# Kernel optimization log

Hardware: AMD Instinct MI355X
Metric: run time of the kernel (lower is better)

## Reference

```python
import jax, jax.numpy as jnp
import numpy as np

LN_EPS = 1e-5

def sin_emb(coords, dim):
    # coords [..., 3] -> [..., dim]; dim split evenly over 3 axes, sin/cos halves
    per_axis = dim // 3
    half = per_axis // 2
    freqs = jnp.exp(-jnp.log(10000.0) * jnp.arange(half, dtype=coords.dtype) / max(half - 1, 1))
    ang = coords[..., None] * freqs  # [..., 3, half]
    emb = jnp.concatenate([jnp.sin(ang), jnp.cos(ang)], axis=-1)  # [..., 3, per_axis]
    return emb.reshape(coords.shape[:-1] + (dim,))

def layernorm(x, g, b):
    mu = jnp.mean(x, axis=-1, keepdims=True)
    var = jnp.mean((x - mu) ** 2, axis=-1, keepdims=True)
    return (x - mu) * jax.lax.rsqrt(var + LN_EPS) * g + b

def point_mlp(x, w, b, g, be, act):
    h = layernorm(x @ w + b, g, be)
    return jax.nn.gelu(h, approximate=False) if act else h

def query_ball_point(radius, nsample, xyz):
    # xyz [B,N,3] -> idx [B,N,nsample] (pad with first in-ball index, PointNet++ style)
    N = xyz.shape[1]
    sq = jnp.sum((xyz[:, :, None, :] - xyz[:, None, :, :]) ** 2, axis=-1)  # [B,N,N]
    idx0 = jnp.where(sq > radius * radius, N, jnp.arange(N)[None, None, :])
    idx = jnp.sort(idx0, axis=-1)[:, :, :nsample]
    return jnp.where(idx == N, idx[:, :, :1], idx)

def index_points(points, idx):
    # points [B,N,C], idx [B,S,K] -> [B,S,K,C]
    return jax.vmap(lambda p, i: p[i])(points, idx)

def setup_inputs() -> dict:
    key = jax.random.key(0)
    ks = jax.random.split(key, 20)
    B, N, C_stem, C_tok = 4, 4096, 64, 256
    C_in = C_stem + 3 + 24 + 96  # 187
    w = lambda k, i, o: jax.random.normal(k, (i, o), jnp.float32) * 0.02
    inp = {
        'xyz': jax.random.uniform(ks[0], (B, N, 3), jnp.float32),
        'point_feature': jax.random.normal(ks[1], (B, N, C_stem), jnp.float32),
        # scene_point_mlp
        'w1': w(ks[2], C_in, C_tok), 'b1': jnp.zeros((C_tok,)), 'g1': jnp.ones((C_tok,)), 'be1': jnp.zeros((C_tok,)),
        'w2': w(ks[3], C_tok, C_tok), 'b2': jnp.zeros((C_tok,)), 'g2': jnp.ones((C_tok,)), 'be2': jnp.zeros((C_tok,)),
        # scene_projection
        'pw1': w(ks[4], C_tok, C_tok), 'pb1': jnp.zeros((C_tok,)), 'pg1': jnp.ones((C_tok,)), 'pbe1': jnp.zeros((C_tok,)),
        'pw2': w(ks[5], C_tok, C_tok), 'pb2': jnp.zeros((C_tok,)), 'pg2': jnp.ones((C_tok,)), 'pbe2': jnp.zeros((C_tok,)),
    }
    return inp

def reference(xyz, point_feature, w1, b1, g1, be1, w2, b2, g2, be2,
              pw1, pb1, pg1, pbe1, pw2, pb2, pg2, pbe2):
    radius, K = 0.16, 32
    idx = query_ball_point(radius, K, xyz)                     # [B,N,K]
    grouped_xyz = index_points(xyz, idx)                       # [B,N,K,3]
    grouped_feature = index_points(point_feature, idx)         # [B,N,K,Cs]
    relative_xyz = grouped_xyz - xyz[:, :, None, :]            # [B,N,K,3]
    relative_position = sin_emb(relative_xyz, 24)              # [B,N,K,24]
    absolute_position = sin_emb(xyz, 96)                       # [B,N,96]
    B, N = xyz.shape[0], xyz.shape[1]
    absolute_position = jnp.broadcast_to(absolute_position[:, :, None, :], (B, N, K, 96))
    grouped_input = jnp.concatenate(
        (grouped_feature, relative_xyz, relative_position, absolute_position), axis=-1)
    h = point_mlp(grouped_input, w1, b1, g1, be1, True)
    h = point_mlp(h, w2, b2, g2, be2, False)
    scene_point_feature = jnp.max(h, axis=2)                   # [B,N,C]
    pooled = jnp.max(scene_point_feature, axis=1, keepdims=True)  # [B,1,C]
    t = point_mlp(pooled, pw1, pb1, pg1, pbe1, True)
    global_scene_token = point_mlp(t, pw2, pb2, pg2, pbe2, False)
    return global_scene_token
```

## Files before the change

### kernel.cpp

```cpp
#include <hip/hip_runtime.h>
#include <math.h>


#define LN_EPS 1e-5f

typedef __attribute__((ext_vector_type(8))) short bf16x8;
typedef __attribute__((ext_vector_type(4))) float f32x4;
typedef __attribute__((ext_vector_type(2))) unsigned int u32x2;
typedef __attribute__((ext_vector_type(4))) unsigned int u32x4;

#if __has_builtin(__builtin_amdgcn_rcpf)
#define FRCP(x) __builtin_amdgcn_rcpf(x)
#else
#define FRCP(x) (1.0f / (x))
#endif

__device__ __forceinline__ unsigned short f2bf(float f) {
    unsigned int x = __float_as_uint(f);
    return (unsigned short)((x + 0x7FFFu + ((x >> 16) & 1u)) >> 16);
}
__device__ __forceinline__ unsigned int pack2(float a, float b) {
    unsigned int ua = __float_as_uint(a), ub = __float_as_uint(b);
    ua = ua + 0x7FFFu + ((ua >> 16) & 1u);
    ub = ub + 0x7FFFu + ((ub >> 16) & 1u);
    return (ua >> 16) | (ub & 0xFFFF0000u);
}
__device__ __forceinline__ unsigned int fenc(float f) {
    unsigned int u = __float_as_uint(f);
    return (u & 0x80000000u) ? ~u : (u | 0x80000000u);
}
__device__ __forceinline__ float fdec(unsigned int u) {
    return __uint_as_float((u & 0x80000000u) ? (u & 0x7FFFFFFFu) : ~u);
}
__device__ __forceinline__ float gelu_fast(float x) {
    float x2 = x * x;
    float u = x * fmaf(0.0356774081f, x2, 0.7978845608f);
    float e = exp2f(u * 2.8853900818f);
    float r = FRCP(e + 1.0f);
    float th = fmaf(-2.0f, r, 1.0f);
    float hx = 0.5f * x;
    return fmaf(hx, th, hx);
}
template<int CTRL>
__device__ __forceinline__ float dppadd(float s) {
    int v = __builtin_amdgcn_update_dpp(0, __float_as_int(s), CTRL, 0xF, 0xF, true);
    return s + __int_as_float(v);
}
__device__ __forceinline__ float rowsum16(float x) {
    x = dppadd<0x128>(x);
    x = dppadd<0x124>(x);
    x = dppadd<0x122>(x);
    x = dppadd<0x121>(x);
    return x;
}

__global__ __launch_bounds__(256) void k_prep(
    const float* __restrict__ w1, const float* __restrict__ w2,
    unsigned short* __restrict__ w2T, unsigned short* __restrict__ w1T,
    unsigned int* __restrict__ pooled, int* __restrict__ done)
{
    int t = threadIdx.x, blk = blockIdx.x;
    if (blk < 16) {
        __shared__ unsigned short tile[64][65];
        int tr = blk >> 2, tc = blk & 3;
        #pragma unroll
        for (int rr = 0; rr < 16; ++rr) {
            int kl = rr * 4 + (t >> 6), nl = t & 63;
            tile[kl][nl] = f2bf(w2[(size_t)(tr * 64 + kl) * 256 + tc * 64 + nl]);
        }
        __syncthreads();
        #pragma unroll
        for (int rr = 0; rr < 16; ++rr) {
            int nl = rr * 4 + (t >> 6), kp = t & 63;
            int kl = (kp & 3) * 16 + (kp >> 2);
            w2T[(size_t)(tc * 64 + nl) * 256 + tr * 64 + kp] = tile[kl][nl];
        }
    } else if (blk < 28) {
        __shared__ unsigned short tile[64][65];
        int idx = blk - 16;
        int tr = idx >> 2, tc = idx & 3;
        #pragma unroll
        for (int rr = 0; rr < 16; ++rr) {
            int kl = rr * 4 + (t >> 6), nl = t & 63;
            int kp = tr * 64 + kl;
            float v = 0.f;
            if (kp < 91)                       v = w1[(size_t)kp * 256 + tc * 64 + nl];
            else if (kp >= 92 && kp <= 187)    v = w1[(size_t)(kp - 1) * 256 + tc * 64 + nl];
            tile[kl][nl] = f2bf(v);
        }
        __syncthreads();
        #pragma unroll
        for (int rr = 0; rr < 16; ++rr) {
            int nl = rr * 4 + (t >> 6), kl = t & 63;
            w1T[(size_t)(tc * 64 + nl) * 192 + tr * 64 + kl] = tile[kl][nl];
        }
    } else {
        unsigned int idv = fenc(-1e19f);
        for (int q = t; q < 1024; q += 256) pooled[q] = idv;
        if (t == 0) *done = 0;
    }
}

__global__ __launch_bounds__(256, 4) void k_main(
    const float* __restrict__ xyz, const float* __restrict__ pf,
    const unsigned short* __restrict__ w1T, const unsigned short* __restrict__ w2T,
    const float* __restrict__ b1, const float* __restrict__ g1,
    const float* __restrict__ be1,
    const float* __restrict__ b2, const float* __restrict__ g2,
    const float* __restrict__ be2,
    unsigned int* __restrict__ pooled, int* __restrict__ done,
    const float* __restrict__ pw1, const float* __restrict__ pb1,
    const float* __restrict__ pg1, const float* __restrict__ pbe1,
    const float* __restrict__ pw2, const float* __restrict__ pb2,
    const float* __restrict__ pg2, const float* __restrict__ pbe2,
    float* __restrict__ out)
{
    __shared__ __align__(16) unsigned short smem[64 * 264];
    __shared__ float embs[2][96];
    __shared__ float reds[64][4][2];
    __shared__ float musig[64][2];
    __shared__ int   idxs[64];
    __shared__ float ctr[2][3];
    __shared__ unsigned long long bmask[2][64];
    __shared__ int   lastf;
    unsigned short* a1s = smem;
    unsigned short* h1s = smem;

    const int N = 4096;
    int tid = threadIdx.x, wv = tid >> 6, lane = tid & 63;
    int lo16 = lane & 15, quad = lane >> 4;
    int b = blockIdx.x & 3;
    int i0 = (blockIdx.x >> 2) * 2;
    size_t base = (size_t)b * N;
    const float* xb = xyz + base * 3;

    bf16x8 bfr0[4], bfr1[4];
    #pragma unroll
    for (int nt = 0; nt < 4; ++nt) {
        int n = wv * 64 + nt * 16 + lo16;
        bfr0[nt] = *(const bf16x8*)&w1T[n * 192 + 0 * 32 + quad * 8];
        bfr1[nt] = *(const bf16x8*)&w1T[n * 192 + 1 * 32 + quad * 8];
    }

    if (tid < 6) { int p = tid / 3, a = tid - 3 * p; ctr[p][a] = xb[(i0 + p) * 3 + a]; }
    if (tid < 192) {
        int p = (tid >= 96) ? 1 : 0, cc = tid - 96 * p;
        int a = cc >> 5, wI = cc & 31;
        int jf = (wI < 16) ? wI : (wI - 16);
        float coord = xb[(i0 + p) * 3 + a];
        float fr = __expf(-0.61402269146507894f * (float)jf);
        float ang = coord * fr;
        embs[p][cc] = (wI < 16) ? __sinf(ang) : __cosf(ang);
    }
    {
        int p = wv >> 1, half = wv & 1;
        float cx = xb[(i0 + p) * 3], cy = xb[(i0 + p) * 3 + 1], cz = xb[(i0 + p) * 3 + 2];
        #pragma unroll 4
        for (int i = 0; i < 32; ++i) {
            int chunk = half * 32 + i;
            int j = chunk * 64 + lane;
            float dx = __fsub_rn(xb[j * 3], cx);
            float dy = __fsub_rn(xb[j * 3 + 1], cy);
            float dz = __fsub_rn(xb[j * 3 + 2], cz);
            float sq = __fadd_rn(__fadd_rn(__fmul_rn(dx, dx), __fmul_rn(dy, dy)),
                                 __fmul_rn(dz, dz));
            bool inball = !((double)sq > (double)0.16 * 0.16);
            unsigned long long m = __ballot(inball);
            if (lane == 0) bmask[p][chunk] = m;
        }
    }
    __syncthreads();
    if (wv < 2) {
        int p = wv;
        unsigned long long m = bmask[p][lane];
        int c = __popcll(m);
        int inc = c;
        #pragma unroll
        for (int d = 1; d <= 32; d <<= 1) {
            int v = __shfl_up(inc, d);
            if (lane >= d) inc += v;
        }
        int exc = inc - c;
        int total = __shfl(inc, 63);
        unsigned long long lm = __ballot(m != 0ull);
        int fl = __ffsll(lm) - 1;
        unsigned long long mf = (unsigned long long)__shfl((long long)m, fl);
        int firstj = fl * 64 + __ffsll(mf) - 1;
        unsigned long long mm = m;
        int t = 0;
        while (mm != 0ull && (exc + t) < 32) {
            int bpos = __ffsll(mm) - 1;
            idxs[p * 32 + exc + t] = lane * 64 + bpos;
            mm &= mm - 1; ++t;
        }
        if (lane >= total && lane < 32) idxs[p * 32 + lane] = firstj;
    }
    __syncthreads();

    {
        int r = tid >> 2, seg = tid & 3;
        int j = idxs[r] & 4095;
        const f32x4* src = (const f32x4*)(pf + (base + (size_t)j) * 64 + seg * 16);
        f32x4 v0 = src[0], v1 = src[1], v2 = src[2], v3 = src[3];
        u32x4 o0, o1;
        o0.x = pack2(v0.x, v0.y); o0.y = pack2(v0.z, v0.w);
        o0.z = pack2(v1.x, v1.y); o0.w = pack2(v1.z, v1.w);
        o1.x = pack2(v2.x, v2.y); o1.y = pack2(v2.z, v2.w);
        o1.z = pack2(v3.x, v3.y); o1.w = pack2(v3.z, v3.w);
        u32x4* dst = (u32x4*)&a1s[r * 200 + seg * 16];
        dst[0] = o0; dst[1] = o1;
    }
    {
        int r = tid & 63, part = tid >> 6;
        int p = r >> 5;
        int j = idxs[r] & 4095;
        float rx = xb[j * 3]     - ctr[p][0];
        float ry = xb[j * 3 + 1] - ctr[p][1];
        float rz = xb[j * 3 + 2] - ctr[p][2];
        unsigned short* arow = &a1s[r * 200];
        if (part == 0) {
            arow[64] = f2bf(rx); arow[65] = f2bf(ry); arow[66] = f2bf(rz);
            arow[91] = 0;
            *(u32x2*)&arow[188] = (u32x2){0u, 0u};
        } else {
            int a = part - 1;
            float cv = (a == 0) ? rx : ((a == 1) ? ry : rz);
            const float fr4[4] = {1.f, 0.046415888336127774f,
                                  0.0021544346900318843f, 1e-4f};
            #pragma unroll
            for (int tt = 0; tt < 4; ++tt) {
                float ang = cv * fr4[tt];
                arow[67 + a * 8 + tt]     = f2bf(__sinf(ang));
                arow[67 + a * 8 + 4 + tt] = f2bf(__cosf(ang));
            }
        }
    }
    {
        int r = tid >> 2, part = tid & 3, p = r >> 5;
        const float* e = embs[p] + part * 24;
        unsigned int* dst = (unsigned int*)&a1s[r * 200 + 92 + part * 24];
        #pragma unroll
        for (int q = 0; q < 12; ++q) dst[q] = pack2(e[2 * q], e[2 * q + 1]);
    }
    __syncthreads();

    f32x4 acc[4][4];
    {
        float b1f[4];
        #pragma unroll
        for (int nt = 0; nt < 4; ++nt) b1f[nt] = b1[wv * 64 + nt * 16 + lo16];
        #pragma unroll
        for (int mt = 0; mt < 4; ++mt)
            #pragma unroll
            for (int nt = 0; nt < 4; ++nt)
                #pragma unroll
                for (int reg = 0; reg < 4; ++reg) acc[mt][nt][reg] = b1f[nt];
    }
    #pragma unroll
    for (int mt = 0; mt < 4; ++mt) {
        bf16x8 afr = *(const bf16x8*)&a1s[(mt * 16 + lo16) * 200 + 0 * 32 + quad * 8];
        #pragma unroll
        for (int nt = 0; nt < 4; ++nt)
            acc[mt][nt] = __builtin_amdgcn_mfma_f32_16x16x32_bf16(
                afr, bfr0[nt], acc[mt][nt], 0, 0, 0);
    }
    #pragma unroll
    for (int mt = 0; mt < 4; ++mt) {
        bf16x8 afr = *(const bf16x8*)&a1s[(mt * 16 + lo16) * 200 + 1 * 32 + quad * 8];
        #pragma unroll
        for (int nt = 0; nt < 4; ++nt)
            acc[mt][nt] = __builtin_amdgcn_mfma_f32_16x16x32_bf16(
                afr, bfr1[nt], acc[mt][nt], 0, 0, 0);
    }
    for (int ks = 2; ks < 6; ++ks) {
        bf16x8 bfr[4];
        #pragma unroll
        for (int nt = 0; nt < 4; ++nt) {
            int n = wv * 64 + nt * 16 + lo16;
            bfr[nt] = *(const bf16x8*)&w1T[n * 192 + ks * 32 + quad * 8];
        }
        #pragma unroll
        for (int mt = 0; mt < 4; ++mt) {
            bf16x8 afr = *(const bf16x8*)&a1s[(mt * 16 + lo16) * 200 + ks * 32 + quad * 8];
            #pragma unroll
            for (int nt = 0; nt < 4; ++nt)
                acc[mt][nt] = __builtin_amdgcn_mfma_f32_16x16x32_bf16(
                    afr, bfr[nt], acc[mt][nt], 0, 0, 0);
        }
    }

    #pragma unroll
    for (int mt = 0; mt < 4; ++mt) {
        #pragma unroll
        for (int reg = 0; reg < 4; ++reg) {
            float s1 = 0.f, s2 = 0.f;
            #pragma unroll
            for (int nt = 0; nt < 4; ++nt) { float v = acc[mt][nt][reg]; s1 += v; s2 = fmaf(v, v, s2); }
            s1 = rowsum16(s1); s2 = rowsum16(s2);
            if (lo16 == 0) { int r = mt * 16 + quad * 4 + reg; reds[r][wv][0] = s1; reds[r][wv][1] = s2; }
        }
    }
    __syncthreads();
    if (tid < 64) {
        int r = tid;
        float s1 = reds[r][0][0] + reds[r][1][0] + reds[r][2][0] + reds[r][3][0];
        float s2 = reds[r][0][1] + reds[r][1][1] + reds[r][2][1] + reds[r][3][1];
        float mu = s1 * (1.f / 256.f);
        float var = fmaxf(s2 * (1.f / 256.f) - mu * mu, 0.f);
        musig[r][0] = mu; musig[r][1] = rsqrtf(var + LN_EPS);
    }
    __syncthreads();
    {
        float g1f[4], be1f[4];
        #pragma unroll
        for (int nt = 0; nt < 4; ++nt) {
            int n = wv * 64 + nt * 16 + lo16;
            g1f[nt] = g1[n]; be1f[nt] = be1[n];
        }
        #pragma unroll
        for (int mt = 0; mt < 4; ++mt) {
            #pragma unroll
            for (int reg = 0; reg < 4; ++reg) {
                int r = mt * 16 + quad * 4 + reg;
                float mu = musig[r][0], rs = musig[r][1];
                float v0 = gelu_fast(fmaf((acc[mt][0][reg] - mu) * rs, g1f[0], be1f[0]));
                float v1 = gelu_fast(fmaf((acc[mt][1][reg] - mu) * rs, g1f[1], be1f[1]));
                float v2 = gelu_fast(fmaf((acc[mt][2][reg] - mu) * rs, g1f[2], be1f[2]));
                float v3 = gelu_fast(fmaf((acc[mt][3][reg] - mu) * rs, g1f[3], be1f[3]));
                u32x2 w; w.x = pack2(v0, v1); w.y = pack2(v2, v3);
                *(u32x2*)&h1s[r * 264 + wv * 64 + lo16 * 4] = w;
            }
        }
    }
    __syncthreads();

    {
        float b2f[4];
        #pragma unroll
        for (int nt = 0; nt < 4; ++nt) b2f[nt] = b2[wv * 64 + nt * 16 + lo16];
        #pragma unroll
        for (int mt = 0; mt < 4; ++mt)
            #pragma unroll
            for (int nt = 0; nt < 4; ++nt)
                #pragma unroll
                for (int reg = 0; reg < 4; ++reg) acc[mt][nt][reg] = b2f[nt];
    }
    for (int ks = 0; ks < 8; ++ks) {
        bf16x8 bfr[4], afr[4];
        #pragma unroll
        for (int nt = 0; nt < 4; ++nt) {
            int n = wv * 64 + nt * 16 + lo16;
            bfr[nt] = *(const bf16x8*)&w2T[n * 256 + ks * 32 + quad * 8];
        }
        #pragma unroll
        for (int mt = 0; mt < 4; ++mt)
            afr[mt] = *(const bf16x8*)&h1s[(mt * 16 + lo16) * 264 + ks * 32 + quad * 8];
        #pragma unroll
        for (int mt = 0; mt < 4; ++mt)
            #pragma unroll
            for (int nt = 0; nt < 4; ++nt)
                acc[mt][nt] = __builtin_amdgcn_mfma_f32_16x16x32_bf16(
                    afr[mt], bfr[nt], acc[mt][nt], 0, 0, 0);
    }

    {
        #pragma unroll
        for (int mt = 0; mt < 4; ++mt) {
            #pragma unroll
            for (int reg = 0; reg < 4; ++reg) {
                float s1 = 0.f, s2 = 0.f;
                #pragma unroll
                for (int nt = 0; nt < 4; ++nt) { float v = acc[mt][nt][reg]; s1 += v; s2 = fmaf(v, v, s2); }
                s1 = rowsum16(s1); s2 = rowsum16(s2);
                if (lo16 == 0) { int r = mt * 16 + quad * 4 + reg; reds[r][wv][0] = s1; reds[r][wv][1] = s2; }
            }
        }
        __syncthreads();
        if (tid < 64) {
            int r = tid;
            float s1 = reds[r][0][0] + reds[r][1][0] + reds[r][2][0] + reds[r][3][0];
            float s2 = reds[r][0][1] + reds[r][1][1] + reds[r][2][1] + reds[r][3][1];
            float mu = s1 * (1.f / 256.f);
            float var = fmaxf(s2 * (1.f / 256.f) - mu * mu, 0.f);
            musig[r][0] = mu; musig[r][1] = rsqrtf(var + LN_EPS);
        }
        __syncthreads();

        float g2f[4], be2f[4];
        #pragma unroll
        for (int nt = 0; nt < 4; ++nt) {
            int n = wv * 64 + nt * 16 + lo16;
            g2f[nt] = g2[n]; be2f[nt] = be2[n];
        }
        float mx[4] = {-1e30f, -1e30f, -1e30f, -1e30f};
        #pragma unroll
        for (int mt = 0; mt < 4; ++mt) {
            #pragma unroll
            for (int reg = 0; reg < 4; ++reg) {
                int r = mt * 16 + quad * 4 + reg;
                float mu = musig[r][0], rs = musig[r][1];
                #pragma unroll
                for (int nt = 0; nt < 4; ++nt) {
                    float v = fmaf((acc[mt][nt][reg] - mu) * rs, g2f[nt], be2f[nt]);
                    mx[nt] = fmaxf(mx[nt], v);
                }
            }
        }
        #pragma unroll
        for (int nt = 0; nt < 4; ++nt) {
            mx[nt] = fmaxf(mx[nt], __shfl_xor(mx[nt], 16));
            mx[nt] = fmaxf(mx[nt], __shfl_xor(mx[nt], 32));
        }
        if (quad == 0) {
            #pragma unroll
            for (int nt = 0; nt < 4; ++nt)
                atomicMax(pooled + b * 256 + wv * 64 + nt * 16 + lo16, fenc(mx[nt]));
        }
    }

    __syncthreads();
    if (tid == 0) lastf = (atomicAdd(done, 1) == 8191);
    __syncthreads();
    if (!lastf) return;
    {
        int bb = wv;
        float* xw = (float*)smem + wv * 512;
        #pragma unroll
        for (int q = 0; q < 4; ++q)
            xw[q * 64 + lane] =
                fdec(atomicMax(&pooled[bb * 256 + q * 64 + lane], 0u));

        float a1[4];
        #pragma unroll
        for (int q = 0; q < 4; ++q) a1[q] = pb1[q * 64 + lane];
        #pragma unroll 4
        for (int k = 0; k < 256; ++k) {
            float xv = xw[k];
            const float* wr = pw1 + (size_t)k * 256 + lane;
            #pragma unroll
            for (int q = 0; q < 4; ++q) a1[q] = fmaf(xv, wr[q * 64], a1[q]);
        }
        float s1 = a1[0] + a1[1] + a1[2] + a1[3];
        float s2 = fmaf(a1[0], a1[0], fmaf(a1[1], a1[1],
                   fmaf(a1[2], a1[2], a1[3] * a1[3])));
        s1 = rowsum16(s1); s2 = rowsum16(s2);
        s1 += __shfl_xor(s1, 16); s2 += __shfl_xor(s2, 16);
        s1 += __shfl_xor(s1, 32); s2 += __shfl_xor(s2, 32);
        float mu = s1 * (1.f / 256.f);
        float rs = rsqrtf(fmaxf(s2 * (1.f / 256.f) - mu * mu, 0.f) + LN_EPS);
        #pragma unroll
        for (int q = 0; q < 4; ++q) {
            int c = q * 64 + lane;
            xw[256 + c] = gelu_fast(fmaf((a1[q] - mu) * rs, pg1[c], pbe1[c]));
        }

        float a2[4];
        #pragma unroll
        for (int q = 0; q < 4; ++q) a2[q] = pb2[q * 64 + lane];
        #pragma unroll 4
        for (int k = 0; k < 256; ++k) {
            float xv = xw[256 + k];
            const float* wr = pw2 + (size_t)k * 256 + lane;
            #pragma unroll
            for (int q = 0; q < 4; ++q) a2[q] = fmaf(xv, wr[q * 64], a2[q]);
        }
        s1 = a2[0] + a2[1] + a2[2] + a2[3];
        s2 = fmaf(a2[0], a2[0], fmaf(a2[1], a2[1],
             fmaf(a2[2], a2[2], a2[3] * a2[3])));
        s1 = rowsum16(s1); s2 = rowsum16(s2);
        s1 += __shfl_xor(s1, 16); s2 += __shfl_xor(s2, 16);
        s1 += __shfl_xor(s1, 32); s2 += __shfl_xor(s2, 32);
        mu = s1 * (1.f / 256.f);
        rs = rsqrtf(fmaxf(s2 * (1.f / 256.f) - mu * mu, 0.f) + LN_EPS);
        #pragma unroll
        for (int q = 0; q < 4; ++q) {
            int c = q * 64 + lane;
            out[bb * 256 + c] = fmaf((a2[q] - mu) * rs, pg2[c], pbe2[c]);
        }
    }
}

extern "C" void kernel_launch(void* const* d_in, const int* in_sizes, int n_in,
                              void* d_out, int out_size, void* d_ws, size_t ws_size,
                              hipStream_t stream)
{
    char* ws = (char*)d_ws;
    unsigned short* w2T    = (unsigned short*)ws;
    unsigned short* w1T    = (unsigned short*)(ws + (128u << 10));
    unsigned int*   pooled = (unsigned int*)(ws + (224u << 10));
    int*            done   = (int*)(ws + (228u << 10));

    k_prep<<<29, 256, 0, stream>>>((const float*)d_in[2], (const float*)d_in[6],
                                   w2T, w1T, pooled, done);
    k_main<<<8192, 256, 0, stream>>>((const float*)d_in[0], (const float*)d_in[1],
                                     w1T, w2T,
                                     (const float*)d_in[3], (const float*)d_in[4],
                                     (const float*)d_in[5],
                                     (const float*)d_in[7], (const float*)d_in[8],
                                     (const float*)d_in[9], pooled, done,
                                     (const float*)d_in[10], (const float*)d_in[11],
                                     (const float*)d_in[12], (const float*)d_in[13],
                                     (const float*)d_in[14], (const float*)d_in[15],
                                     (const float*)d_in[16], (const float*)d_in[17],
                                     (float*)d_out);
}
```

Before: 457.7 us.

## Give each wave full-row MFMA tiles to keep LayerNorm in registers

Each wave now owns 16 full rows across all 256 output columns instead of a 64-column slice of all 64 rows. LayerNorm row statistics can then be reduced inside the wave, which removes the cross-wave shared-memory reductions and several block barriers. Per-channel bias, gamma and beta are staged once in LDS, the double-precision radius compare becomes a float threshold compare, and the per-wave maxima are merged in LDS so each block issues one atomic per channel. In exchange every wave loads the full weight matrices from global/L2 with no register reuse of B fragments across row tiles, which raises weight traffic fourfold and may increase register pressure.

```diff
diff --git a/kernel.cpp b/kernel.cpp
--- a/kernel.cpp
+++ b/kernel.cpp
@@ -116,15 +116,15 @@
     float* __restrict__ out)
 {
     __shared__ __align__(16) unsigned short smem[64 * 264];
-    __shared__ float embs[2][96];
-    __shared__ float reds[64][4][2];
-    __shared__ float musig[64][2];
+    __shared__ __align__(16) char aux[6 * 256 * 4];
     __shared__ int   idxs[64];
     __shared__ float ctr[2][3];
-    __shared__ unsigned long long bmask[2][64];
     __shared__ int   lastf;
     unsigned short* a1s = smem;
     unsigned short* h1s = smem;
+    float* embs  = (float*)aux;
+    unsigned long long* bmask = (unsigned long long*)(aux + 768);
+    float* consts = (float*)aux;
 
     const int N = 4096;
     int tid = threadIdx.x, wv = tid >> 6, lane = tid & 63;
@@ -133,14 +133,6 @@
     int i0 = (blockIdx.x >> 2) * 2;
     size_t base = (size_t)b * N;
     const float* xb = xyz + base * 3;
-
-    bf16x8 bfr0[4], bfr1[4];
-    #pragma unroll
-    for (int nt = 0; nt < 4; ++nt) {
-        int n = wv * 64 + nt * 16 + lo16;
-        bfr0[nt] = *(const bf16x8*)&w1T[n * 192 + 0 * 32 + quad * 8];
-        bfr1[nt] = *(const bf16x8*)&w1T[n * 192 + 1 * 32 + quad * 8];
-    }
 
     if (tid < 6) { int p = tid / 3, a = tid - 3 * p; ctr[p][a] = xb[(i0 + p) * 3 + a]; }
     if (tid < 192) {
@@ -150,8 +142,11 @@
         float coord = xb[(i0 + p) * 3 + a];
         float fr = __expf(-0.61402269146507894f * (float)jf);
         float ang = coord * fr;
-        embs[p][cc] = (wI < 16) ? __sinf(ang) : __cosf(ang);
-    }
+        embs[p * 96 + cc] = (wI < 16) ? __sinf(ang) : __cosf(ang);
+    }
+    const double r2d = 0.16 * 0.16;
+    float T = (float)r2d;
+    if ((double)T > r2d) T = __uint_as_float(__float_as_uint(T) - 1u);
     {
         int p = wv >> 1, half = wv & 1;
         float cx = xb[(i0 + p) * 3], cy = xb[(i0 + p) * 3 + 1], cz = xb[(i0 + p) * 3 + 2];
@@ -164,15 +159,15 @@
             float dz = __fsub_rn(xb[j * 3 + 2], cz);
             float sq = __fadd_rn(__fadd_rn(__fmul_rn(dx, dx), __fmul_rn(dy, dy)),
                                  __fmul_rn(dz, dz));
-            bool inball = !((double)sq > (double)0.16 * 0.16);
+            bool inball = (sq <= T);
             unsigned long long m = __ballot(inball);
-            if (lane == 0) bmask[p][chunk] = m;
+            if (lane == 0) bmask[p * 64 + chunk] = m;
         }
     }
     __syncthreads();
     if (wv < 2) {
         int p = wv;
-        unsigned long long m = bmask[p][lane];
+        unsigned long long m = bmask[p * 64 + lane];
         int c = __popcll(m);
         int inc = c;
         #pragma unroll
@@ -237,185 +232,140 @@
     }
     {
         int r = tid >> 2, part = tid & 3, p = r >> 5;
-        const float* e = embs[p] + part * 24;
+        const float* e = embs + p * 96 + part * 24;
         unsigned int* dst = (unsigned int*)&a1s[r * 200 + 92 + part * 24];
         #pragma unroll
         for (int q = 0; q < 12; ++q) dst[q] = pack2(e[2 * q], e[2 * q + 1]);
     }
     __syncthreads();
 
-    f32x4 acc[4][4];
-    {
-        float b1f[4];
-        #pragma unroll
-        for (int nt = 0; nt < 4; ++nt) b1f[nt] = b1[wv * 64 + nt * 16 + lo16];
-        #pragma unroll
-        for (int mt = 0; mt < 4; ++mt)
-            #pragma unroll
-            for (int nt = 0; nt < 4; ++nt)
-                #pragma unroll
-                for (int reg = 0; reg < 4; ++reg) acc[mt][nt][reg] = b1f[nt];
-    }
+    {
+        int t = tid;
+        int pos = (t >> 6) * 64 + (t & 15) * 4 + ((t >> 4) & 3);
+        consts[0 * 256 + pos] = b1[t];  consts[1 * 256 + pos] = g1[t];
+        consts[2 * 256 + pos] = be1[t]; consts[3 * 256 + pos] = b2[t];
+        consts[4 * 256 + pos] = g2[t];  consts[5 * 256 + pos] = be2[t];
+    }
+    __syncthreads();
+
+    f32x4 acc[16];
     #pragma unroll
-    for (int mt = 0; mt < 4; ++mt) {
-        bf16x8 afr = *(const bf16x8*)&a1s[(mt * 16 + lo16) * 200 + 0 * 32 + quad * 8];
-        #pragma unroll
-        for (int nt = 0; nt < 4; ++nt)
-            acc[mt][nt] = __builtin_amdgcn_mfma_f32_16x16x32_bf16(
-                afr, bfr0[nt], acc[mt][nt], 0, 0, 0);
-    }
+    for (int c64 = 0; c64 < 4; ++c64) {
+        f32x4 bv = *(const f32x4*)&consts[0 * 256 + c64 * 64 + lo16 * 4];
+        #pragma unroll
+        for (int ntp = 0; ntp < 4; ++ntp) {
+            float v = bv[ntp];
+            acc[c64 * 4 + ntp] = (f32x4){v, v, v, v};
+        }
+    }
+    for (int ks = 0; ks < 6; ++ks) {
+        bf16x8 afr = *(const bf16x8*)&a1s[(wv * 16 + lo16) * 200 + ks * 32 + quad * 8];
+        #pragma unroll
+        for (int nt = 0; nt < 16; ++nt) {
+            bf16x8 bfr = *(const bf16x8*)&w1T[(nt * 16 + lo16) * 192 + ks * 32 + quad * 8];
+            acc[nt] = __builtin_amdgcn_mfma_f32_16x16x32_bf16(afr, bfr, acc[nt], 0, 0, 0);
+        }
+    }
+
+    float mu4[4], rs4[4];
     #pragma unroll
-    for (int mt = 0; mt < 4; ++mt) {
-        bf16x8 afr = *(const bf16x8*)&a1s[(mt * 16 + lo16) * 200 + 1 * 32 + quad * 8];
-        #pragma unroll
-        for (int nt = 0; nt < 4; ++nt)
-            acc[mt][nt] = __builtin_amdgcn_mfma_f32_16x16x32_bf16(
-                afr, bfr1[nt], acc[mt][nt], 0, 0, 0);
-    }
-    for (int ks = 2; ks < 6; ++ks) {
-        bf16x8 bfr[4];
-        #pragma unroll
-        for (int nt = 0; nt < 4; ++nt) {
-            int n = wv * 64 + nt * 16 + lo16;
-            bfr[nt] = *(const bf16x8*)&w1T[n * 192 + ks * 32 + quad * 8];
-        }
-        #pragma unroll
-        for (int mt = 0; mt < 4; ++mt) {
-            bf16x8 afr = *(const bf16x8*)&a1s[(mt * 16 + lo16) * 200 + ks * 32 + quad * 8];
-            #pragma unroll
-            for (int nt = 0; nt < 4; ++nt)
-                acc[mt][nt] = __builtin_amdgcn_mfma_f32_16x16x32_bf16(
-                    afr, bfr[nt], acc[mt][nt], 0, 0, 0);
-        }
-    }
-
-    #pragma unroll
-    for (int mt = 0; mt < 4; ++mt) {
-        #pragma unroll
-        for (int reg = 0; reg < 4; ++reg) {
-            float s1 = 0.f, s2 = 0.f;
-            #pragma unroll
-            for (int nt = 0; nt < 4; ++nt) { float v = acc[mt][nt][reg]; s1 += v; s2 = fmaf(v, v, s2); }
-            s1 = rowsum16(s1); s2 = rowsum16(s2);
-            if (lo16 == 0) { int r = mt * 16 + quad * 4 + reg; reds[r][wv][0] = s1; reds[r][wv][1] = s2; }
-        }
-    }
-    __syncthreads();
-    if (tid < 64) {
-        int r = tid;
-        float s1 = reds[r][0][0] + reds[r][1][0] + reds[r][2][0] + reds[r][3][0];
-        float s2 = reds[r][0][1] + reds[r][1][1] + reds[r][2][1] + reds[r][3][1];
+    for (int reg = 0; reg < 4; ++reg) {
+        float s1 = 0.f, s2 = 0.f;
+        #pragma unroll
+        for (int nt = 0; nt < 16; ++nt) { float v = acc[nt][reg]; s1 += v; s2 = fmaf(v, v, s2); }
+        s1 = rowsum16(s1); s2 = rowsum16(s2);
         float mu = s1 * (1.f / 256.f);
         float var = fmaxf(s2 * (1.f / 256.f) - mu * mu, 0.f);
-        musig[r][0] = mu; musig[r][1] = rsqrtf(var + LN_EPS);
-    }
-    __syncthreads();
-    {
-        float g1f[4], be1f[4];
-        #pragma unroll
-        for (int nt = 0; nt < 4; ++nt) {
-            int n = wv * 64 + nt * 16 + lo16;
-            g1f[nt] = g1[n]; be1f[nt] = be1[n];
-        }
-        #pragma unroll
-        for (int mt = 0; mt < 4; ++mt) {
+        mu4[reg] = mu; rs4[reg] = rsqrtf(var + LN_EPS);
+    }
+    __syncthreads();
+    {
+        int rowb = (wv * 16 + quad * 4) * 264;
+        #pragma unroll
+        for (int c64 = 0; c64 < 4; ++c64) {
+            f32x4 g1q = *(const f32x4*)&consts[1 * 256 + c64 * 64 + lo16 * 4];
+            f32x4 e1q = *(const f32x4*)&consts[2 * 256 + c64 * 64 + lo16 * 4];
             #pragma unroll
             for (int reg = 0; reg < 4; ++reg) {
-                int r = mt * 16 + quad * 4 + reg;
-                float mu = musig[r][0], rs = musig[r][1];
-                float v0 = gelu_fast(fmaf((acc[mt][0][reg] - mu) * rs, g1f[0], be1f[0]));
-                float v1 = gelu_fast(fmaf((acc[mt][1][reg] - mu) * rs, g1f[1], be1f[1]));
-                float v2 = gelu_fast(fmaf((acc[mt][2][reg] - mu) * rs, g1f[2], be1f[2]));
-                float v3 = gelu_fast(fmaf((acc[mt][3][reg] - mu) * rs, g1f[3], be1f[3]));
+                float mu = mu4[reg], rs = rs4[reg];
+                float v0 = gelu_fast(fmaf((acc[c64 * 4 + 0][reg] - mu) * rs, g1q.x, e1q.x));
+                float v1 = gelu_fast(fmaf((acc[c64 * 4 + 1][reg] - mu) * rs, g1q.y, e1q.y));
+                float v2 = gelu_fast(fmaf((acc[c64 * 4 + 2][reg] - mu) * rs, g1q.z, e1q.z));
+                float v3 = gelu_fast(fmaf((acc[c64 * 4 + 3][reg] - mu) * rs, g1q.w, e1q.w));
                 u32x2 w; w.x = pack2(v0, v1); w.y = pack2(v2, v3);
-                *(u32x2*)&h1s[r * 264 + wv * 64 + lo16 * 4] = w;
+                *(u32x2*)&h1s[rowb + reg * 264 + c64 * 64 + lo16 * 4] = w;
             }
         }
     }
-    __syncthreads();
-
-    {
-        float b2f[4];
-        #pragma unroll
-        for (int nt = 0; nt < 4; ++nt) b2f[nt] = b2[wv * 64 + nt * 16 + lo16];
-        #pragma unroll
-        for (int mt = 0; mt < 4; ++mt)
-            #pragma unroll
-            for (int nt = 0; nt < 4; ++nt)
+
+    #pragma unroll
+    for (int c64 = 0; c64 < 4; ++c64) {
+        f32x4 bv = *(const f32x4*)&consts[3 * 256 + c64 * 64 + lo16 * 4];
+        #pragma unroll
+        for (int ntp = 0; ntp < 4; ++ntp) {
+            float v = bv[ntp];
+            acc[c64 * 4 + ntp] = (f32x4){v, v, v, v};
+        }
+    }
+    for (int ks = 0; ks < 8; ++ks) {
+        bf16x8 afr = *(const bf16x8*)&h1s[(wv * 16 + lo16) * 264 + ks * 32 + quad * 8];
+        #pragma unroll
+        for (int nt = 0; nt < 16; ++nt) {
+            bf16x8 bfr = *(const bf16x8*)&w2T[(nt * 16 + lo16) * 256 + ks * 32 + quad * 8];
+            acc[nt] = __builtin_amdgcn_mfma_f32_16x16x32_bf16(afr, bfr, acc[nt], 0, 0, 0);
+        }
+    }
+
+    #pragma unroll
+    for (int reg = 0; reg < 4; ++reg) {
+        float s1 = 0.f, s2 = 0.f;
+        #pragma unroll
+        for (int nt = 0; nt < 16; ++nt) { float v = acc[nt][reg]; s1 += v; s2 = fmaf(v, v, s2); }
+        s1 = rowsum16(s1); s2 = rowsum16(s2);
+        float mu = s1 * (1.f / 256.f);
+        float var = fmaxf(s2 * (1.f / 256.f) - mu * mu, 0.f);
+        mu4[reg] = mu; rs4[reg] = rsqrtf(var + LN_EPS);
+    }
+    {
+        float mxv[16];
+        #pragma unroll
+        for (int nt = 0; nt < 16; ++nt) mxv[nt] = -1e30f;
+        #pragma unroll
+        for (int c64 = 0; c64 < 4; ++c64) {
+            f32x4 g2q = *(const f32x4*)&consts[4 * 256 + c64 * 64 + lo16 * 4];
+            f32x4 e2q = *(const f32x4*)&consts[5 * 256 + c64 * 64 + lo16 * 4];
+            #pragma unroll
+            for (int ntp = 0; ntp < 4; ++ntp) {
+                float gv = g2q[ntp], ev = e2q[ntp];
+                float m = mxv[c64 * 4 + ntp];
                 #pragma unroll
-                for (int reg = 0; reg < 4; ++reg) acc[mt][nt][reg] = b2f[nt];
-    }
-    for (int ks = 0; ks < 8; ++ks) {
-        bf16x8 bfr[4], afr[4];
-        #pragma unroll
-        for (int nt = 0; nt < 4; ++nt) {
-            int n = wv * 64 + nt * 16 + lo16;
-            bfr[nt] = *(const bf16x8*)&w2T[n * 256 + ks * 32 + quad * 8];
-        }
-        #pragma unroll
-        for (int mt = 0; mt < 4; ++mt)
-            afr[mt] = *(const bf16x8*)&h1s[(mt * 16 + lo16) * 264 + ks * 32 + quad * 8];
-        #pragma unroll
-        for (int mt = 0; mt < 4; ++mt)
-            #pragma unroll
-            for (int nt = 0; nt < 4; ++nt)
-                acc[mt][nt] = __builtin_amdgcn_mfma_f32_16x16x32_bf16(
-                    afr[mt], bfr[nt], acc[mt][nt], 0, 0, 0);
-    }
-
-    {
-        #pragma unroll
-        for (int mt = 0; mt < 4; ++mt) {
-            #pragma unroll
-            for (int reg = 0; reg < 4; ++reg) {
-                float s1 = 0.f, s2 = 0.f;
-                #pragma unroll
-                for (int nt = 0; nt < 4; ++nt) { float v = acc[mt][nt][reg]; s1 += v; s2 = fmaf(v, v, s2); }
-                s1 = rowsum16(s1); s2 = rowsum16(s2);
-                if (lo16 == 0) { int r = mt * 16 + quad * 4 + reg; reds[r][wv][0] = s1; reds[r][wv][1] = s2; }
+                for (int reg = 0; reg < 4; ++reg) {
+                    float v = fmaf((acc[c64 * 4 + ntp][reg] - mu4[reg]) * rs4[reg], gv, ev);
+                    m = fmaxf(m, v);
+                }
+                mxv[c64 * 4 + ntp] = m;
             }
         }
-        __syncthreads();
-        if (tid < 64) {
-            int r = tid;
-            float s1 = reds[r][0][0] + reds[r][1][0] + reds[r][2][0] + reds[r][3][0];
-            float s2 = reds[r][0][1] + reds[r][1][1] + reds[r][2][1] + reds[r][3][1];
-            float mu = s1 * (1.f / 256.f);
-            float var = fmaxf(s2 * (1.f / 256.f) - mu * mu, 0.f);
-            musig[r][0] = mu; musig[r][1] = rsqrtf(var + LN_EPS);
-        }
-        __syncthreads();
-
-        float g2f[4], be2f[4];
-        #pragma unroll
-        for (int nt = 0; nt < 4; ++nt) {
-            int n = wv * 64 + nt * 16 + lo16;
-            g2f[nt] = g2[n]; be2f[nt] = be2[n];
-        }
-        float mx[4] = {-1e30f, -1e30f, -1e30f, -1e30f};
-        #pragma unroll
-        for (int mt = 0; mt < 4; ++mt) {
-            #pragma unroll
-            for (int reg = 0; reg < 4; ++reg) {
-                int r = mt * 16 + quad * 4 + reg;
-                float mu = musig[r][0], rs = musig[r][1];
-                #pragma unroll
-                for (int nt = 0; nt < 4; ++nt) {
-                    float v = fmaf((acc[mt][nt][reg] - mu) * rs, g2f[nt], be2f[nt]);
-                    mx[nt] = fmaxf(mx[nt], v);
-                }
-            }
-        }
-        #pragma unroll
-        for (int nt = 0; nt < 4; ++nt) {
-            mx[nt] = fmaxf(mx[nt], __shfl_xor(mx[nt], 16));
-            mx[nt] = fmaxf(mx[nt], __shfl_xor(mx[nt], 32));
-        }
+        #pragma unroll
+        for (int nt = 0; nt < 16; ++nt) {
+            mxv[nt] = fmaxf(mxv[nt], __shfl_xor(mxv[nt], 16));
+            mxv[nt] = fmaxf(mxv[nt], __shfl_xor(mxv[nt], 32));
+        }
+        float* lmx = (float*)&smem[wv * 16 * 264];
         if (quad == 0) {
             #pragma unroll
-            for (int nt = 0; nt < 4; ++nt)
-                atomicMax(pooled + b * 256 + wv * 64 + nt * 16 + lo16, fenc(mx[nt]));
-        }
+            for (int nt = 0; nt < 16; ++nt) lmx[nt * 16 + lo16] = mxv[nt];
+        }
+    }
+    __syncthreads();
+    {
+        int t = tid;
+        float m0 = ((float*)&smem[0 * 16 * 264])[t];
+        float m1 = ((float*)&smem[1 * 16 * 264])[t];
+        float m2 = ((float*)&smem[2 * 16 * 264])[t];
+        float m3 = ((float*)&smem[3 * 16 * 264])[t];
+        float m = fmaxf(fmaxf(m0, m1), fmaxf(m2, m3));
+        atomicMax(pooled + b * 256 + t, fenc(m));
     }
 
     __syncthreads();
```

Result: slower. 1.026 ms (+124.1%).

## Process one query point per block and raise occupancy to six blocks

Applied to the files above, without the earlier changes.

Each block now handles a single centre point (32 neighbour rows) instead of two, which doubles the grid to 16384 blocks and halves shared memory and accumulator registers. The launch bound is raised from 4 to 6 blocks per SM. Other changes: the ball-query scan is split across all four waves, the absolute embedding is pre-packed to bf16 once per block, and a float threshold replaces the double compare. The cost is that every block reloads the w1/w2 fragments for only half the rows, so weight reuse per MFMA drops and there are more per-block fixed overheads and atomics.

```diff
diff --git a/kernel.cpp b/kernel.cpp
--- a/kernel.cpp
+++ b/kernel.cpp
@@ -1,4 +1,5 @@
 #include <hip/hip_runtime.h>
+#include <hip/hip_bf16.h>
 #include <math.h>
 
 
@@ -20,10 +21,9 @@
     return (unsigned short)((x + 0x7FFFu + ((x >> 16) & 1u)) >> 16);
 }
 __device__ __forceinline__ unsigned int pack2(float a, float b) {
-    unsigned int ua = __float_as_uint(a), ub = __float_as_uint(b);
-    ua = ua + 0x7FFFu + ((ua >> 16) & 1u);
-    ub = ub + 0x7FFFu + ((ub >> 16) & 1u);
-    return (ua >> 16) | (ub & 0xFFFF0000u);
+    union { __hip_bfloat162 h; unsigned int u; } cvt;
+    cvt.h = __float22bfloat162_rn(make_float2(a, b));
+    return cvt.u;
 }
 __device__ __forceinline__ unsigned int fenc(float f) {
     unsigned int u = __float_as_uint(f);
@@ -101,7 +101,7 @@
     }
 }
 
-__global__ __launch_bounds__(256, 4) void k_main(
+__global__ __launch_bounds__(256, 6) void k_main(
     const float* __restrict__ xyz, const float* __restrict__ pf,
     const unsigned short* __restrict__ w1T, const unsigned short* __restrict__ w2T,
     const float* __restrict__ b1, const float* __restrict__ g1,
@@ -115,13 +115,13 @@
     const float* __restrict__ pg2, const float* __restrict__ pbe2,
     float* __restrict__ out)
 {
-    __shared__ __align__(16) unsigned short smem[64 * 264];
-    __shared__ float embs[2][96];
-    __shared__ float reds[64][4][2];
-    __shared__ float musig[64][2];
-    __shared__ int   idxs[64];
-    __shared__ float ctr[2][3];
-    __shared__ unsigned long long bmask[2][64];
+    __shared__ __align__(16) unsigned short smem[32 * 264];
+    __shared__ __align__(16) unsigned int epack[48];
+    __shared__ unsigned long long bmask[64];
+    __shared__ float reds[32][4][2];
+    __shared__ float musig[32][2];
+    __shared__ int   idxs[32];
+    __shared__ float ctr[3];
     __shared__ int   lastf;
     unsigned short* a1s = smem;
     unsigned short* h1s = smem;
@@ -130,49 +130,46 @@
     int tid = threadIdx.x, wv = tid >> 6, lane = tid & 63;
     int lo16 = lane & 15, quad = lane >> 4;
     int b = blockIdx.x & 3;
-    int i0 = (blockIdx.x >> 2) * 2;
+    int i = blockIdx.x >> 2;
     size_t base = (size_t)b * N;
     const float* xb = xyz + base * 3;
 
-    bf16x8 bfr0[4], bfr1[4];
-    #pragma unroll
-    for (int nt = 0; nt < 4; ++nt) {
-        int n = wv * 64 + nt * 16 + lo16;
-        bfr0[nt] = *(const bf16x8*)&w1T[n * 192 + 0 * 32 + quad * 8];
-        bfr1[nt] = *(const bf16x8*)&w1T[n * 192 + 1 * 32 + quad * 8];
-    }
-
-    if (tid < 6) { int p = tid / 3, a = tid - 3 * p; ctr[p][a] = xb[(i0 + p) * 3 + a]; }
-    if (tid < 192) {
-        int p = (tid >= 96) ? 1 : 0, cc = tid - 96 * p;
-        int a = cc >> 5, wI = cc & 31;
-        int jf = (wI < 16) ? wI : (wI - 16);
-        float coord = xb[(i0 + p) * 3 + a];
-        float fr = __expf(-0.61402269146507894f * (float)jf);
-        float ang = coord * fr;
-        embs[p][cc] = (wI < 16) ? __sinf(ang) : __cosf(ang);
-    }
-    {
-        int p = wv >> 1, half = wv & 1;
-        float cx = xb[(i0 + p) * 3], cy = xb[(i0 + p) * 3 + 1], cz = xb[(i0 + p) * 3 + 2];
+    if (tid < 3) ctr[tid] = xb[i * 3 + tid];
+    if (tid < 48) {
+        float vals[2];
+        #pragma unroll
+        for (int q = 0; q < 2; ++q) {
+            int cc = tid * 2 + q;
+            int a = cc >> 5, wI = cc & 31;
+            int jf = (wI < 16) ? wI : (wI - 16);
+            float coord = xb[i * 3 + a];
+            float fr = __expf(-0.61402269146507894f * (float)jf);
+            float ang = coord * fr;
+            vals[q] = (wI < 16) ? __sinf(ang) : __cosf(ang);
+        }
+        epack[tid] = pack2(vals[0], vals[1]);
+    }
+    const double r2d = 0.16 * 0.16;
+    float T = (float)r2d;
+    if ((double)T > r2d) T = __uint_as_float(__float_as_uint(T) - 1u);
+    {
+        float cx = xb[i * 3], cy = xb[i * 3 + 1], cz = xb[i * 3 + 2];
         #pragma unroll 4
-        for (int i = 0; i < 32; ++i) {
-            int chunk = half * 32 + i;
+        for (int it = 0; it < 16; ++it) {
+            int chunk = wv * 16 + it;
             int j = chunk * 64 + lane;
             float dx = __fsub_rn(xb[j * 3], cx);
             float dy = __fsub_rn(xb[j * 3 + 1], cy);
             float dz = __fsub_rn(xb[j * 3 + 2], cz);
             float sq = __fadd_rn(__fadd_rn(__fmul_rn(dx, dx), __fmul_rn(dy, dy)),
                                  __fmul_rn(dz, dz));
-            bool inball = !((double)sq > (double)0.16 * 0.16);
-            unsigned long long m = __ballot(inball);
-            if (lane == 0) bmask[p][chunk] = m;
-        }
-    }
-    __syncthreads();
-    if (wv < 2) {
-        int p = wv;
-        unsigned long long m = bmask[p][lane];
+            unsigned long long m = __ballot(sq <= T);
+            if (lane == 0) bmask[chunk] = m;
+        }
+    }
+    __syncthreads();
+    if (wv == 0) {
+        unsigned long long m = bmask[lane];
         int c = __popcll(m);
         int inc = c;
         #pragma unroll
@@ -190,36 +187,33 @@
         int t = 0;
         while (mm != 0ull && (exc + t) < 32) {
             int bpos = __ffsll(mm) - 1;
-            idxs[p * 32 + exc + t] = lane * 64 + bpos;
+            idxs[exc + t] = lane * 64 + bpos;
             mm &= mm - 1; ++t;
         }
-        if (lane >= total && lane < 32) idxs[p * 32 + lane] = firstj;
-    }
-    __syncthreads();
-
-    {
-        int r = tid >> 2, seg = tid & 3;
-        int j = idxs[r] & 4095;
-        const f32x4* src = (const f32x4*)(pf + (base + (size_t)j) * 64 + seg * 16);
-        f32x4 v0 = src[0], v1 = src[1], v2 = src[2], v3 = src[3];
-        u32x4 o0, o1;
-        o0.x = pack2(v0.x, v0.y); o0.y = pack2(v0.z, v0.w);
-        o0.z = pack2(v1.x, v1.y); o0.w = pack2(v1.z, v1.w);
-        o1.x = pack2(v2.x, v2.y); o1.y = pack2(v2.z, v2.w);
-        o1.z = pack2(v3.x, v3.y); o1.w = pack2(v3.z, v3.w);
-        u32x4* dst = (u32x4*)&a1s[r * 200 + seg * 16];
-        dst[0] = o0; dst[1] = o1;
-    }
-    {
-        int r = tid & 63, part = tid >> 6;
-        int p = r >> 5;
-        int j = idxs[r] & 4095;
-        float rx = xb[j * 3]     - ctr[p][0];
-        float ry = xb[j * 3 + 1] - ctr[p][1];
-        float rz = xb[j * 3 + 2] - ctr[p][2];
+        if (lane >= total && lane < 32) idxs[lane] = firstj;
+    }
+    __syncthreads();
+
+    {
+        int r = tid >> 3, seg = tid & 7;
+        int j = idxs[r];
+        const f32x4* src = (const f32x4*)(pf + (base + (size_t)j) * 64 + seg * 8);
+        f32x4 v0 = src[0], v1 = src[1];
+        u32x4 o;
+        o.x = pack2(v0.x, v0.y); o.y = pack2(v0.z, v0.w);
+        o.z = pack2(v1.x, v1.y); o.w = pack2(v1.z, v1.w);
+        *(u32x4*)&a1s[r * 200 + seg * 8] = o;
+    }
+    if (tid < 128) {
+        int r = tid & 31, part = tid >> 5;
+        int j = idxs[r];
+        float rx = xb[j * 3]     - ctr[0];
+        float ry = xb[j * 3 + 1] - ctr[1];
+        float rz = xb[j * 3 + 2] - ctr[2];
         unsigned short* arow = &a1s[r * 200];
         if (part == 0) {
-            arow[64] = f2bf(rx); arow[65] = f2bf(ry); arow[66] = f2bf(rz);
+            *(unsigned int*)&arow[64] = pack2(rx, ry);
+            arow[66] = f2bf(rz);
             arow[91] = 0;
             *(u32x2*)&arow[188] = (u32x2){0u, 0u};
         } else {
@@ -236,43 +230,26 @@
         }
     }
     {
-        int r = tid >> 2, part = tid & 3, p = r >> 5;
-        const float* e = embs[p] + part * 24;
-        unsigned int* dst = (unsigned int*)&a1s[r * 200 + 92 + part * 24];
-        #pragma unroll
-        for (int q = 0; q < 12; ++q) dst[q] = pack2(e[2 * q], e[2 * q + 1]);
-    }
-    __syncthreads();
-
-    f32x4 acc[4][4];
+        int r = tid >> 3, part = tid & 7;
+        const u32x2* e = (const u32x2*)(epack + part * 6);
+        u32x2* dst = (u32x2*)&a1s[r * 200 + 92 + part * 12];
+        dst[0] = e[0]; dst[1] = e[1]; dst[2] = e[2];
+    }
+    __syncthreads();
+
+    f32x4 acc[2][4];
     {
         float b1f[4];
         #pragma unroll
         for (int nt = 0; nt < 4; ++nt) b1f[nt] = b1[wv * 64 + nt * 16 + lo16];
         #pragma unroll
-        for (int mt = 0; mt < 4; ++mt)
+        for (int mt = 0; mt < 2; ++mt)
             #pragma unroll
             for (int nt = 0; nt < 4; ++nt)
                 #pragma unroll
                 for (int reg = 0; reg < 4; ++reg) acc[mt][nt][reg] = b1f[nt];
     }
-    #pragma unroll
-    for (int mt = 0; mt < 4; ++mt) {
-        bf16x8 afr = *(const bf16x8*)&a1s[(mt * 16 + lo16) * 200 + 0 * 32 + quad * 8];
-        #pragma unroll
-        for (int nt = 0; nt < 4; ++nt)
-            acc[mt][nt] = __builtin_amdgcn_mfma_f32_16x16x32_bf16(
-                afr, bfr0[nt], acc[mt][nt], 0, 0, 0);
-    }
-    #pragma unroll
-    for (int mt = 0; mt < 4; ++mt) {
-        bf16x8 afr = *(const bf16x8*)&a1s[(mt * 16 + lo16) * 200 + 1 * 32 + quad * 8];
-        #pragma unroll
-        for (int nt = 0; nt < 4; ++nt)
-            acc[mt][nt] = __builtin_amdgcn_mfma_f32_16x16x32_bf16(
-                afr, bfr1[nt], acc[mt][nt], 0, 0, 0);
-    }
-    for (int ks = 2; ks < 6; ++ks) {
+    for (int ks = 0; ks < 6; ++ks) {
         bf16x8 bfr[4];
         #pragma unroll
         for (int nt = 0; nt < 4; ++nt) {
@@ -280,7 +257,7 @@
             bfr[nt] = *(const bf16x8*)&w1T[n * 192 + ks * 32 + quad * 8];
         }
         #pragma unroll
-        for (int mt = 0; mt < 4; ++mt) {
+        for (int mt = 0; mt < 2; ++mt) {
             bf16x8 afr = *(const bf16x8*)&a1s[(mt * 16 + lo16) * 200 + ks * 32 + quad * 8];
             #pragma unroll
             for (int nt = 0; nt < 4; ++nt)
@@ -290,7 +267,7 @@
     }
 
     #pragma unroll
-    for (int mt = 0; mt < 4; ++mt) {
+    for (int mt = 0; mt < 2; ++mt) {
         #pragma unroll
         for (int reg = 0; reg < 4; ++reg) {
             float s1 = 0.f, s2 = 0.f;
@@ -301,7 +278,7 @@
         }
     }
     __syncthreads();
-    if (tid < 64) {
+    if (tid < 32) {
         int r = tid;
         float s1 = reds[r][0][0] + reds[r][1][0] + reds[r][2][0] + reds[r][3][0];
         float s2 = reds[r][0][1] + reds[r][1][1] + reds[r][2][1] + reds[r][3][1];
@@ -318,7 +295,7 @@
             g1f[nt] = g1[n]; be1f[nt] = be1[n];
         }
         #pragma unroll
-        for (int mt = 0; mt < 4; ++mt) {
+        for (int mt = 0; mt < 2; ++mt) {
             #pragma unroll
             for (int reg = 0; reg < 4; ++reg) {
                 int r = mt * 16 + quad * 4 + reg;
@@ -339,24 +316,24 @@
         #pragma unroll
         for (int nt = 0; nt < 4; ++nt) b2f[nt] = b2[wv * 64 + nt * 16 + lo16];
         #pragma unroll
-        for (int mt = 0; mt < 4; ++mt)
+        for (int mt = 0; mt < 2; ++mt)
             #pragma unroll
             for (int nt = 0; nt < 4; ++nt)
                 #pragma unroll
                 for (int reg = 0; reg < 4; ++reg) acc[mt][nt][reg] = b2f[nt];
     }
     for (int ks = 0; ks < 8; ++ks) {
-        bf16x8 bfr[4], afr[4];
+        bf16x8 bfr[4], afr[2];
         #pragma unroll
         for (int nt = 0; nt < 4; ++nt) {
             int n = wv * 64 + nt * 16 + lo16;
             bfr[nt] = *(const bf16x8*)&w2T[n * 256 + ks * 32 + quad * 8];
         }
         #pragma unroll
-        for (int mt = 0; mt < 4; ++mt)
+        for (int mt = 0; mt < 2; ++mt)
             afr[mt] = *(const bf16x8*)&h1s[(mt * 16 + lo16) * 264 + ks * 32 + quad * 8];
         #pragma unroll
-        for (int mt = 0; mt < 4; ++mt)
+        for (int mt = 0; mt < 2; ++mt)
             #pragma unroll
             for (int nt = 0; nt < 4; ++nt)
                 acc[mt][nt] = __builtin_amdgcn_mfma_f32_16x16x32_bf16(
@@ -365,7 +342,7 @@
 
     {
         #pragma unroll
-        for (int mt = 0; mt < 4; ++mt) {
+        for (int mt = 0; mt < 2; ++mt) {
             #pragma unroll
             for (int reg = 0; reg < 4; ++reg) {
                 float s1 = 0.f, s2 = 0.f;
@@ -376,7 +353,7 @@
             }
         }
         __syncthreads();
-        if (tid < 64) {
+        if (tid < 32) {
             int r = tid;
             float s1 = reds[r][0][0] + reds[r][1][0] + reds[r][2][0] + reds[r][3][0];
             float s2 = reds[r][0][1] + reds[r][1][1] + reds[r][2][1] + reds[r][3][1];
@@ -394,7 +371,7 @@
         }
         float mx[4] = {-1e30f, -1e30f, -1e30f, -1e30f};
         #pragma unroll
-        for (int mt = 0; mt < 4; ++mt) {
+        for (int mt = 0; mt < 2; ++mt) {
             #pragma unroll
             for (int reg = 0; reg < 4; ++reg) {
                 int r = mt * 16 + quad * 4 + reg;
@@ -419,7 +396,7 @@
     }
 
     __syncthreads();
-    if (tid == 0) lastf = (atomicAdd(done, 1) == 8191);
+    if (tid == 0) lastf = (atomicAdd(done, 1) == 16383);
     __syncthreads();
     if (!lastf) return;
     {
@@ -492,15 +469,15 @@
 
     k_prep<<<29, 256, 0, stream>>>((const float*)d_in[2], (const float*)d_in[6],
                                    w2T, w1T, pooled, done);
-    k_main<<<8192, 256, 0, stream>>>((const float*)d_in[0], (const float*)d_in[1],
-                                     w1T, w2T,
-                                     (const float*)d_in[3], (const float*)d_in[4],
-                                     (const float*)d_in[5],
-                                     (const float*)d_in[7], (const float*)d_in[8],
-                                     (const float*)d_in[9], pooled, done,
-                                     (const float*)d_in[10], (const float*)d_in[11],
-                                     (const float*)d_in[12], (const float*)d_in[13],
-                                     (const float*)d_in[14], (const float*)d_in[15],
-                                     (const float*)d_in[16], (const float*)d_in[17],
-                                     (float*)d_out);
-}
+    k_main<<<16384, 256, 0, stream>>>((const float*)d_in[0], (const float*)d_in[1],
+                                      w1T, w2T,
+                                      (const float*)d_in[3], (const float*)d_in[4],
+                                      (const float*)d_in[5],
+                                      (const float*)d_in[7], (const float*)d_in[8],
+                                      (const float*)d_in[9], pooled, done,
+                                      (const float*)d_in[10], (const float*)d_in[11],
+                                      (const float*)d_in[12], (const float*)d_in[13],
+                                      (const float*)d_in[14], (const float*)d_in[15],
+                                      (const float*)d_in[16], (const float*)d_in[17],
+                                      (float*)d_out);
+}
```

Result: slower. 602.2 us (+31.6%).
